# Kernel optimization log

Measured on AMD Instinct MI355X. Metric: run time of the kernel, lower is better.

## Reference

```python
import jax, jax.numpy as jnp
import numpy as np

T = 2048        # sequence length
E = 1024        # embedding_dim
H = 1024        # hidden_dim
V = 50257       # vocab_size
TAGS = 50       # tagset_size


def setup_inputs() -> dict:
    key = jax.random.key(0)
    ks = jax.random.split(key, 8)
    s = 1.0 / np.sqrt(H)
    return {
        "sentence": jax.random.randint(ks[0], (T,), 0, V, dtype=jnp.int64),
        "emb": jax.random.normal(ks[1], (V, E), dtype=jnp.float32),
        "W_ih": jax.random.uniform(ks[2], (3 * H, E), jnp.float32, -s, s),
        "W_hh": jax.random.uniform(ks[3], (3 * H, H), jnp.float32, -s, s),
        "b_ih": jax.random.uniform(ks[4], (3 * H,), jnp.float32, -s, s),
        "b_hh": jax.random.uniform(ks[5], (3 * H,), jnp.float32, -s, s),
        "W_out": jax.random.uniform(ks[6], (TAGS, H), jnp.float32, -s, s),
        "b_out": jax.random.uniform(ks[7], (TAGS,), jnp.float32, -s, s),
    }


def _gru_scan(x, W_ih, W_hh, b_ih, b_hh):
    # x: [T, E]. Precompute all input-side gate projections in one GEMM.
    gi_all = x @ W_ih.T + b_ih            # [T, 3H]
    W_hhT = W_hh.T                         # [H, 3H]
    h0 = jnp.zeros((W_hh.shape[1],), x.dtype)

    def step(h, gi):
        gh = h @ W_hhT + b_hh              # [3H]
        i_r, i_z, i_n = jnp.split(gi, 3)
        h_r, h_z, h_n = jnp.split(gh, 3)
        r = jax.nn.sigmoid(i_r + h_r)
        z = jax.nn.sigmoid(i_z + h_z)
        n = jnp.tanh(i_n + r * h_n)
        h_new = (1.0 - z) * n + z * h
        return h_new, h_new

    _, hs = jax.lax.scan(step, h0, gi_all)  # hs: [T, H]
    return hs


def reference(sentence, emb, W_ih, W_hh, b_ih, b_hh, W_out, b_out):
    x = emb[sentence]                       # [T, E] embedding lookup
    hs = _gru_scan(x, W_ih, W_hh, b_ih, b_hh)  # [T, H]
    tag_space = hs @ W_out.T + b_out        # [T, TAGS]
    return jax.nn.log_softmax(tag_space, axis=-1)
```

## Files before the change

kernel.cpp:

```cpp
#include <hip/hip_runtime.h>
#include <hip/hip_bf16.h>


#define T_SEQ 2048
#define E_DIM 1024
#define H_DIM 1024
#define N3H   3072
#define VTAGS 50
#define VOCAB 50257
#define NWG   64
#define IPW   (H_DIM / NWG)
#define SBLK  512

typedef short bf16x8 __attribute__((ext_vector_type(8)));
typedef float f32x4  __attribute__((ext_vector_type(4)));
typedef float f32x2  __attribute__((ext_vector_type(2)));

__device__ inline unsigned short f2bf_rne(float f) {
  unsigned int u = __float_as_uint(f);
  u += 0x7FFFu + ((u >> 16) & 1u);
  return (unsigned short)(u >> 16);
}

__global__ __launch_bounds__(256) void k_gather_cast(
    const int* __restrict__ sent, const float* __restrict__ emb,
    unsigned short* __restrict__ Xb) {
  const int t = blockIdx.x;
  int row = sent[t];
  row = (row < 0) ? 0 : ((row >= VOCAB) ? VOCAB - 1 : row);
  const float4* src = (const float4*)(emb + (size_t)row * E_DIM);
  float4 v = src[threadIdx.x];
  ushort4 o;
  o.x = f2bf_rne(v.x); o.y = f2bf_rne(v.y); o.z = f2bf_rne(v.z); o.w = f2bf_rne(v.w);
  ((ushort4*)(Xb + (size_t)t * E_DIM))[threadIdx.x] = o;
}

__global__ __launch_bounds__(256) void k_cast_w(
    const float* __restrict__ W, unsigned short* __restrict__ Wb) {
  const int r = blockIdx.x;
  const float4* src = (const float4*)(W + (size_t)r * E_DIM);
  float4 v = src[threadIdx.x];
  ushort4 o;
  o.x = f2bf_rne(v.x); o.y = f2bf_rne(v.y); o.z = f2bf_rne(v.z); o.w = f2bf_rne(v.w);
  ((ushort4*)(Wb + (size_t)r * E_DIM))[threadIdx.x] = o;
}

__global__ __launch_bounds__(256) void k_gemm_gi(
    const unsigned short* __restrict__ Xb, const unsigned short* __restrict__ Wb,
    const float* __restrict__ b_ih, float* __restrict__ gi) {
  const int tid = threadIdx.x;
  const int lane = tid & 63;
  const int wv = tid >> 6;
  const int m_base = blockIdx.y * 128 + (wv & 1) * 64;
  const int n_base = blockIdx.x * 128 + (wv >> 1) * 64;
  const int lr = lane & 15;
  const int kq = (lane >> 4) * 8;
  f32x4 acc[4][4] = {};
  for (int k0 = 0; k0 < E_DIM; k0 += 32) {
    bf16x8 a[4], b[4];
#pragma unroll
    for (int mi = 0; mi < 4; ++mi)
      a[mi] = *(const bf16x8*)(Xb + (size_t)(m_base + mi * 16 + lr) * E_DIM + k0 + kq);
#pragma unroll
    for (int ni = 0; ni < 4; ++ni)
      b[ni] = *(const bf16x8*)(Wb + (size_t)(n_base + ni * 16 + lr) * E_DIM + k0 + kq);
#pragma unroll
    for (int mi = 0; mi < 4; ++mi)
#pragma unroll
      for (int ni = 0; ni < 4; ++ni)
        acc[mi][ni] = __builtin_amdgcn_mfma_f32_16x16x32_bf16(a[mi], b[ni], acc[mi][ni], 0, 0, 0);
  }
  const int row_q = (lane >> 4) * 4;
#pragma unroll
  for (int mi = 0; mi < 4; ++mi) {
#pragma unroll
    for (int ni = 0; ni < 4; ++ni) {
      const int col  = n_base + ni * 16 + lr;
      const int row0 = m_base + mi * 16 + row_q;
      const float bv = b_ih[col];
#pragma unroll
      for (int rr = 0; rr < 4; ++rr)
        gi[(size_t)(row0 + rr) * N3H + col] = acc[mi][ni][rr] + bv;
    }
  }
}

__global__ __launch_bounds__(SBLK) __attribute__((amdgpu_waves_per_eu(2, 2)))
void k_gru_scan(const float* __restrict__ W_hh, const float* __restrict__ b_hh,
                const float* __restrict__ gi, float* __restrict__ hs,
                float* data, int* tags) {
  const int wg  = blockIdx.x;
  const int tid = threadIdx.x;
  const int row = tid >> 5;
  const int cg  = tid & 31;
  const int lane = tid & 63;
  const int i   = wg * IPW + row;

  __shared__ float hsh[2][H_DIM];

  f32x4 w0[8], w1[8], w2[8];
  {
    const f32x4* p0 = (const f32x4*)(W_hh + (size_t)i * H_DIM);
    const f32x4* p1 = (const f32x4*)(W_hh + (size_t)(H_DIM + i) * H_DIM);
    const f32x4* p2 = (const f32x4*)(W_hh + (size_t)(2 * H_DIM + i) * H_DIM);
#pragma unroll
    for (int q = 0; q < 8; ++q) {
      w0[q] = p0[cg + q * 32];
      w1[q] = p1[cg + q * 32];
      w2[q] = p2[cg + q * 32];
    }
  }
  const float bh0 = b_hh[i], bh1 = b_hh[H_DIM + i], bh2 = b_hh[2 * H_DIM + i];

  for (int t = 0; t < T_SEQ; ++t) {
    asm volatile("" : "+v"(w0[0]), "+v"(w0[1]), "+v"(w0[2]), "+v"(w0[3]),
                      "+v"(w0[4]), "+v"(w0[5]), "+v"(w0[6]), "+v"(w0[7]),
                      "+v"(w1[0]), "+v"(w1[1]), "+v"(w1[2]), "+v"(w1[3]),
                      "+v"(w1[4]), "+v"(w1[5]), "+v"(w1[6]), "+v"(w1[7]),
                      "+v"(w2[0]), "+v"(w2[1]), "+v"(w2[2]), "+v"(w2[3]),
                      "+v"(w2[4]), "+v"(w2[5]), "+v"(w2[6]), "+v"(w2[7]));

    const float gir = gi[(size_t)t * N3H + i];
    const float giz = gi[(size_t)t * N3H + H_DIM + i];
    const float gin = gi[(size_t)t * N3H + 2 * H_DIM + i];

    if (tid < 64) {
      {
        const int* tp = tags + (size_t)(t & 1) * 64 + lane;
        const unsigned tt = (unsigned)t;
        unsigned v;
        int it = 0;
        while (true) {
          asm volatile("global_load_dword %0, %1, off sc0 sc1\n\ts_waitcnt vmcnt(0)"
                       : "=v"(v) : "v"(tp));
          if (__all(v == tt) || ++it > (1 << 16)) break;
        }
      }
      {
        const float* dp = data + (size_t)(t & 1) * H_DIM + lane * 16;
        f32x4 d0, d1, d2, d3;
        asm volatile(
            "global_load_dwordx4 %0, %4, off sc0 sc1\n\t"
            "global_load_dwordx4 %1, %4, off offset:16 sc0 sc1\n\t"
            "global_load_dwordx4 %2, %4, off offset:32 sc0 sc1\n\t"
            "global_load_dwordx4 %3, %4, off offset:48 sc0 sc1\n\t"
            "s_waitcnt vmcnt(0)"
            : "=v"(d0), "=v"(d1), "=v"(d2), "=v"(d3)
            : "v"(dp));
        f32x4* hb4 = (f32x4*)hsh[t & 1];
        hb4[lane * 4 + 0] = d0;
        hb4[lane * 4 + 1] = d1;
        hb4[lane * 4 + 2] = d2;
        hb4[lane * 4 + 3] = d3;
      }
    }
    __syncthreads();

    const float* hb = hsh[t & 1];
    const f32x4* hb4 = (const f32x4*)hb;
    float a0 = 0.f, a1 = 0.f, a2 = 0.f;
#pragma unroll
    for (int q = 0; q < 8; ++q) {
      f32x4 hv = hb4[cg + q * 32];
      a0 = fmaf(w0[q][0], hv[0], a0); a0 = fmaf(w0[q][1], hv[1], a0);
      a0 = fmaf(w0[q][2], hv[2], a0); a0 = fmaf(w0[q][3], hv[3], a0);
      a1 = fmaf(w1[q][0], hv[0], a1); a1 = fmaf(w1[q][1], hv[1], a1);
      a1 = fmaf(w1[q][2], hv[2], a1); a1 = fmaf(w1[q][3], hv[3], a1);
      a2 = fmaf(w2[q][0], hv[0], a2); a2 = fmaf(w2[q][1], hv[1], a2);
      a2 = fmaf(w2[q][2], hv[2], a2); a2 = fmaf(w2[q][3], hv[3], a2);
    }
#pragma unroll
    for (int off = 16; off >= 1; off >>= 1) {
      a0 += __shfl_xor(a0, off, 64);
      a1 += __shfl_xor(a1, off, 64);
      a2 += __shfl_xor(a2, off, 64);
    }
    const float r = 1.f / (1.f + __expf(-(gir + a0 + bh0)));
    const float z = 1.f / (1.f + __expf(-(giz + a1 + bh1)));
    const float nx = gin + r * (a2 + bh2);
    const float e2 = __expf(-2.f * fabsf(nx));
    float n = (1.f - e2) / (1.f + e2);
    n = (nx < 0.f) ? -n : n;
    const float hold = hb[i];
    const float hnew = (1.f - z) * n + z * hold;

    if (cg == 0) {
      __hip_atomic_store(&data[(size_t)((t + 1) & 1) * H_DIM + i], hnew,
                         __ATOMIC_RELAXED, __HIP_MEMORY_SCOPE_AGENT);
      hs[(size_t)t * H_DIM + i] = hnew;
    }
    __syncthreads();
    if (tid == 0)
      __hip_atomic_store(&tags[(size_t)((t + 1) & 1) * 64 + wg], t + 1,
                         __ATOMIC_RELAXED, __HIP_MEMORY_SCOPE_AGENT);
  }
}

__global__ __launch_bounds__(256) void k_out(
    const float* __restrict__ hs, const float* __restrict__ W_out,
    const float* __restrict__ b_out, float* __restrict__ out) {
  const int t = blockIdx.x;
  const int tid = threadIdx.x;
  const int wv = tid >> 6, lane = tid & 63;
  __shared__ float xs[H_DIM];
  __shared__ float tagv[64];
  ((float4*)xs)[tid] = ((const float4*)(hs + (size_t)t * H_DIM))[tid];
  __syncthreads();
  for (int g = wv; g < VTAGS; g += 4) {
    const float4* wr = (const float4*)(W_out + (size_t)g * H_DIM);
    const float4* xr = (const float4*)xs;
    float s = 0.f;
#pragma unroll
    for (int q = 0; q < 4; ++q) {
      float4 a = wr[lane * 4 + q];
      float4 b = xr[lane * 4 + q];
      s += a.x * b.x + a.y * b.y + a.z * b.z + a.w * b.w;
    }
#pragma unroll
    for (int off = 1; off < 64; off <<= 1) s += __shfl_xor(s, off, 64);
    if (lane == 0) tagv[g] = s + b_out[g];
  }
  __syncthreads();
  if (tid < 64) {
    const float v = (tid < VTAGS) ? tagv[tid] : -1e30f;
    float m = v;
#pragma unroll
    for (int off = 1; off < 64; off <<= 1) m = fmaxf(m, __shfl_xor(m, off, 64));
    float e = (tid < VTAGS) ? __expf(v - m) : 0.f;
    float se = e;
#pragma unroll
    for (int off = 1; off < 64; off <<= 1) se += __shfl_xor(se, off, 64);
    const float lse = logf(se);
    if (tid < VTAGS) out[(size_t)t * VTAGS + tid] = v - m - lse;
  }
}

extern "C" void kernel_launch(void* const* d_in, const int* in_sizes, int n_in,
                              void* d_out, int out_size, void* d_ws, size_t ws_size,
                              hipStream_t stream) {
  const int* sent    = (const int*)d_in[0];
  const float* emb   = (const float*)d_in[1];
  const float* W_ih  = (const float*)d_in[2];
  const float* W_hh  = (const float*)d_in[3];
  const float* b_ih  = (const float*)d_in[4];
  const float* b_hh  = (const float*)d_in[5];
  const float* W_out = (const float*)d_in[6];
  const float* b_out = (const float*)d_in[7];
  float* out = (float*)d_out;

  char* ws = (char*)d_ws;
  const size_t OFF_GI = 0;
  const size_t OFF_B  = (size_t)T_SEQ * N3H * 4;
  const size_t OFF_XB = OFF_B;
  const size_t OFF_WB = OFF_B + (size_t)T_SEQ * E_DIM * 2;
  const size_t OFF_HS = OFF_B;
  const size_t OFF_DT = OFF_B + 10485760;
  const size_t OFF_TG = OFF_DT + 2 * H_DIM * 4;
  const size_t NEED = OFF_TG + 2 * 64 * 4;
  if (ws_size < NEED) return;

  float* gi = (float*)(ws + OFF_GI);
  unsigned short* Xb = (unsigned short*)(ws + OFF_XB);
  unsigned short* Wb = (unsigned short*)(ws + OFF_WB);
  float* hs = (float*)(ws + OFF_HS);
  float* data = (float*)(ws + OFF_DT);
  int* tags = (int*)(ws + OFF_TG);

  hipMemsetAsync(ws + OFF_DT, 0, 2 * H_DIM * 4 + 2 * 64 * 4, stream);

  k_gather_cast<<<T_SEQ, 256, 0, stream>>>(sent, emb, Xb);
  k_cast_w<<<N3H, 256, 0, stream>>>(W_ih, Wb);
  k_gemm_gi<<<dim3(N3H / 128, T_SEQ / 128), 256, 0, stream>>>(Xb, Wb, b_ih, gi);
  k_gru_scan<<<NWG, SBLK, 0, stream>>>(W_hh, b_hh, gi, hs, data, tags);
  k_out<<<T_SEQ, 256, 0, stream>>>(hs, W_out, b_out, out);
}
```

Before: 5.687 ms.

## Add dedicated poller wave and replace second barrier with LDS counter publish

The scan block gains a 9th wave that only polls the cross-workgroup tags and copies the hidden state into LDS, while the 8 compute waves hold the W_hh rows in registers. The second __syncthreads per step is dropped: each compute wave publishes its slice, then bumps a shared-memory counter, and the last wave to arrive writes the global tag. The hs store and the gi loads move to the next iteration so they sit off the critical path. The aim is to shorten per-step latency in the serial recurrence, at the cost of an extra wave per block, a different occupancy setting, and more delicate memory-ordering logic.

```diff
diff --git a/kernel.cpp b/kernel.cpp
--- a/kernel.cpp
+++ b/kernel.cpp
@@ -10,11 +10,10 @@
 #define VOCAB 50257
 #define NWG   64
 #define IPW   (H_DIM / NWG)
-#define SBLK  512
+#define SBLK  576
 
 typedef short bf16x8 __attribute__((ext_vector_type(8)));
 typedef float f32x4  __attribute__((ext_vector_type(4)));
-typedef float f32x2  __attribute__((ext_vector_type(2)));
 
 __device__ inline unsigned short f2bf_rne(float f) {
   unsigned int u = __float_as_uint(f);
@@ -85,21 +84,26 @@
   }
 }
 
-__global__ __launch_bounds__(SBLK) __attribute__((amdgpu_waves_per_eu(2, 2)))
+__global__ __launch_bounds__(SBLK) __attribute__((amdgpu_waves_per_eu(3, 3)))
 void k_gru_scan(const float* __restrict__ W_hh, const float* __restrict__ b_hh,
                 const float* __restrict__ gi, float* __restrict__ hs,
                 float* data, int* tags) {
   const int wg  = blockIdx.x;
   const int tid = threadIdx.x;
-  const int row = tid >> 5;
-  const int cg  = tid & 31;
+  const bool poller = (tid < 64);
   const int lane = tid & 63;
+  const int ctid = poller ? 0 : (tid - 64);
+  const int row = ctid >> 5;
+  const int cg  = ctid & 31;
   const int i   = wg * IPW + row;
 
   __shared__ float hsh[2][H_DIM];
+  __shared__ int cnt[2];
+  if (tid == 0) { cnt[0] = 0; cnt[1] = 0; }
 
   f32x4 w0[8], w1[8], w2[8];
-  {
+  float bh0 = 0.f, bh1 = 0.f, bh2 = 0.f;
+  if (!poller) {
     const f32x4* p0 = (const f32x4*)(W_hh + (size_t)i * H_DIM);
     const f32x4* p1 = (const f32x4*)(W_hh + (size_t)(H_DIM + i) * H_DIM);
     const f32x4* p2 = (const f32x4*)(W_hh + (size_t)(2 * H_DIM + i) * H_DIM);
@@ -109,22 +113,14 @@
       w1[q] = p1[cg + q * 32];
       w2[q] = p2[cg + q * 32];
     }
-  }
-  const float bh0 = b_hh[i], bh1 = b_hh[H_DIM + i], bh2 = b_hh[2 * H_DIM + i];
+    bh0 = b_hh[i]; bh1 = b_hh[H_DIM + i]; bh2 = b_hh[2 * H_DIM + i];
+  }
+
+  float hnew = 0.f;
+  float gir = 0.f, giz = 0.f, gin = 0.f;
 
   for (int t = 0; t < T_SEQ; ++t) {
-    asm volatile("" : "+v"(w0[0]), "+v"(w0[1]), "+v"(w0[2]), "+v"(w0[3]),
-                      "+v"(w0[4]), "+v"(w0[5]), "+v"(w0[6]), "+v"(w0[7]),
-                      "+v"(w1[0]), "+v"(w1[1]), "+v"(w1[2]), "+v"(w1[3]),
-                      "+v"(w1[4]), "+v"(w1[5]), "+v"(w1[6]), "+v"(w1[7]),
-                      "+v"(w2[0]), "+v"(w2[1]), "+v"(w2[2]), "+v"(w2[3]),
-                      "+v"(w2[4]), "+v"(w2[5]), "+v"(w2[6]), "+v"(w2[7]));
-
-    const float gir = gi[(size_t)t * N3H + i];
-    const float giz = gi[(size_t)t * N3H + H_DIM + i];
-    const float gin = gi[(size_t)t * N3H + 2 * H_DIM + i];
-
-    if (tid < 64) {
+    if (poller) {
       {
         const int* tp = tags + (size_t)(t & 1) * 64 + lane;
         const unsigned tt = (unsigned)t;
@@ -153,47 +149,69 @@
         hb4[lane * 4 + 2] = d2;
         hb4[lane * 4 + 3] = d3;
       }
-    }
+    } else {
+      if (t > 0) {
+        if (cg == 0)
+          __hip_atomic_store(&data[(size_t)(t & 1) * H_DIM + i], hnew,
+                             __ATOMIC_RELAXED, __HIP_MEMORY_SCOPE_AGENT);
+        asm volatile("s_waitcnt vmcnt(0)" ::: "memory");
+        if ((ctid & 63) == 0) {
+          int old = __hip_atomic_fetch_add(&cnt[t & 1], 1, __ATOMIC_RELAXED,
+                                           __HIP_MEMORY_SCOPE_WORKGROUP);
+          if (old == 7) {
+            cnt[t & 1] = 0;
+            __hip_atomic_store(&tags[(size_t)(t & 1) * 64 + wg], t,
+                               __ATOMIC_RELAXED, __HIP_MEMORY_SCOPE_AGENT);
+          }
+        }
+        if (cg == 0)
+          hs[(size_t)(t - 1) * H_DIM + i] = hnew;
+      }
+      gir = gi[(size_t)t * N3H + i];
+      giz = gi[(size_t)t * N3H + H_DIM + i];
+      gin = gi[(size_t)t * N3H + 2 * H_DIM + i];
+      asm volatile("" : "+v"(w0[0]), "+v"(w0[1]), "+v"(w0[2]), "+v"(w0[3]),
+                        "+v"(w0[4]), "+v"(w0[5]), "+v"(w0[6]), "+v"(w0[7]),
+                        "+v"(w1[0]), "+v"(w1[1]), "+v"(w1[2]), "+v"(w1[3]),
+                        "+v"(w1[4]), "+v"(w1[5]), "+v"(w1[6]), "+v"(w1[7]),
+                        "+v"(w2[0]), "+v"(w2[1]), "+v"(w2[2]), "+v"(w2[3]),
+                        "+v"(w2[4]), "+v"(w2[5]), "+v"(w2[6]), "+v"(w2[7]));
+    }
+
     __syncthreads();
 
-    const float* hb = hsh[t & 1];
-    const f32x4* hb4 = (const f32x4*)hb;
-    float a0 = 0.f, a1 = 0.f, a2 = 0.f;
-#pragma unroll
-    for (int q = 0; q < 8; ++q) {
-      f32x4 hv = hb4[cg + q * 32];
-      a0 = fmaf(w0[q][0], hv[0], a0); a0 = fmaf(w0[q][1], hv[1], a0);
-      a0 = fmaf(w0[q][2], hv[2], a0); a0 = fmaf(w0[q][3], hv[3], a0);
-      a1 = fmaf(w1[q][0], hv[0], a1); a1 = fmaf(w1[q][1], hv[1], a1);
-      a1 = fmaf(w1[q][2], hv[2], a1); a1 = fmaf(w1[q][3], hv[3], a1);
-      a2 = fmaf(w2[q][0], hv[0], a2); a2 = fmaf(w2[q][1], hv[1], a2);
-      a2 = fmaf(w2[q][2], hv[2], a2); a2 = fmaf(w2[q][3], hv[3], a2);
-    }
-#pragma unroll
-    for (int off = 16; off >= 1; off >>= 1) {
-      a0 += __shfl_xor(a0, off, 64);
-      a1 += __shfl_xor(a1, off, 64);
-      a2 += __shfl_xor(a2, off, 64);
-    }
-    const float r = 1.f / (1.f + __expf(-(gir + a0 + bh0)));
-    const float z = 1.f / (1.f + __expf(-(giz + a1 + bh1)));
-    const float nx = gin + r * (a2 + bh2);
-    const float e2 = __expf(-2.f * fabsf(nx));
-    float n = (1.f - e2) / (1.f + e2);
-    n = (nx < 0.f) ? -n : n;
-    const float hold = hb[i];
-    const float hnew = (1.f - z) * n + z * hold;
-
-    if (cg == 0) {
-      __hip_atomic_store(&data[(size_t)((t + 1) & 1) * H_DIM + i], hnew,
-                         __ATOMIC_RELAXED, __HIP_MEMORY_SCOPE_AGENT);
-      hs[(size_t)t * H_DIM + i] = hnew;
-    }
-    __syncthreads();
-    if (tid == 0)
-      __hip_atomic_store(&tags[(size_t)((t + 1) & 1) * 64 + wg], t + 1,
-                         __ATOMIC_RELAXED, __HIP_MEMORY_SCOPE_AGENT);
-  }
+    if (!poller) {
+      const float* hb = hsh[t & 1];
+      const f32x4* hb4 = (const f32x4*)hb;
+      float a0 = 0.f, a1 = 0.f, a2 = 0.f;
+#pragma unroll
+      for (int q = 0; q < 8; ++q) {
+        f32x4 hv = hb4[cg + q * 32];
+        a0 = fmaf(w0[q][0], hv[0], a0); a0 = fmaf(w0[q][1], hv[1], a0);
+        a0 = fmaf(w0[q][2], hv[2], a0); a0 = fmaf(w0[q][3], hv[3], a0);
+        a1 = fmaf(w1[q][0], hv[0], a1); a1 = fmaf(w1[q][1], hv[1], a1);
+        a1 = fmaf(w1[q][2], hv[2], a1); a1 = fmaf(w1[q][3], hv[3], a1);
+        a2 = fmaf(w2[q][0], hv[0], a2); a2 = fmaf(w2[q][1], hv[1], a2);
+        a2 = fmaf(w2[q][2], hv[2], a2); a2 = fmaf(w2[q][3], hv[3], a2);
+      }
+#pragma unroll
+      for (int off = 16; off >= 1; off >>= 1) {
+        a0 += __shfl_xor(a0, off, 64);
+        a1 += __shfl_xor(a1, off, 64);
+        a2 += __shfl_xor(a2, off, 64);
+      }
+      const float r = 1.f / (1.f + __expf(-(gir + a0 + bh0)));
+      const float z = 1.f / (1.f + __expf(-(giz + a1 + bh1)));
+      const float nx = gin + r * (a2 + bh2);
+      const float e2 = __expf(-2.f * fabsf(nx));
+      float n = (1.f - e2) / (1.f + e2);
+      n = (nx < 0.f) ? -n : n;
+      const float hold = hb[i];
+      hnew = (1.f - z) * n + z * hold;
+    }
+  }
+  if (!poller && cg == 0)
+    hs[(size_t)(T_SEQ - 1) * H_DIM + i] = hnew;
 }
 
 __global__ __launch_bounds__(256) void k_out(
@@ -266,7 +284,7 @@
   float* data = (float*)(ws + OFF_DT);
   int* tags = (int*)(ws + OFF_TG);
 
-  hipMemsetAsync(ws + OFF_DT, 0, 2 * H_DIM * 4 + 2 * 64 * 4, stream);
+  (void)hipMemsetAsync(ws + OFF_DT, 0, 2 * H_DIM * 4 + 2 * 64 * 4, stream);
 
   k_gather_cast<<<T_SEQ, 256, 0, stream>>>(sent, emb, Xb);
   k_cast_w<<<N3H, 256, 0, stream>>>(W_ih, Wb);
```

After: 8.818 ms. 1.55x slower.
